# Kernel tuning notes

Measured on AMD Instinct MI355X. Metric: run time of the kernel, lower is better.

## Reference

```python
import jax, jax.numpy as jnp
import numpy as np

B, S = 2, 2048
DIM_IN, DIM_OUT, NUM_HEADS, DIM_QK = 1024, 128, 16, 128


def setup_inputs() -> dict:
    key = jax.random.key(0)
    k0, k1, k2, k3 = jax.random.split(key, 4)
    x = jax.random.normal(k0, (B, S, DIM_IN), jnp.float32)
    mask = jax.random.bernoulli(k1, 0.1, (B, S))  # True = masked-out token
    # xavier-normal-ish scales (exact init values are irrelevant for correctness)
    std_in = float(np.sqrt(2.0 / (NUM_HEADS * DIM_QK + DIM_IN * DIM_QK)))
    proj_in = jax.random.normal(k2, (DIM_IN, NUM_HEADS, 2 * DIM_QK + DIM_OUT), jnp.float32) * std_in
    v_bias = jnp.zeros((NUM_HEADS, DIM_OUT), jnp.float32)
    std_out = float(np.sqrt(2.0 / (DIM_OUT * DIM_OUT + NUM_HEADS * DIM_OUT)))
    proj_out = jax.random.normal(k3, (NUM_HEADS, DIM_OUT, DIM_OUT), jnp.float32) * std_out
    proj_out_bias = jnp.zeros((DIM_OUT,), jnp.float32)
    return {"x": x, "mask": mask, "proj_in": proj_in, "v_bias": v_bias,
            "proj_out": proj_out, "proj_out_bias": proj_out_bias}


def _rotary(t):
    # t: [z, s, h, d]; GPT-NeoX style rotary as in the torch Rotary module
    d = t.shape[-1]
    half = -(-d // 2)  # ceil(d/2), matches torch.arange(0,-1,-2/d)
    freq_half = 10000.0 ** (jnp.arange(half, dtype=jnp.float32) * (-2.0 / d))
    freq = jnp.concatenate([freq_half, freq_half[: half - d % 2]])  # length d
    pos = jnp.arange(t.shape[1], dtype=jnp.float32)
    ang = pos[:, None] * freq[None, :]             # [s, d]
    cos = jnp.cos(ang)[None, :, None, :]
    sin = jnp.sin(ang)[None, :, None, :]
    x1, x2 = jnp.split(t, 2, axis=-1)
    rot = jnp.concatenate([-x2, x1], axis=-1)
    return t * cos + rot * sin


def _inf_cube(t):
    return t ** 3


def reference(x, mask, proj_in, v_bias, proj_out, proj_out_bias):
    qkv = jnp.einsum('zki,iho->zkho', x, proj_in)
    q, k, v = jnp.split(qkv, [DIM_QK, 2 * DIM_QK], axis=-1)
    q = _rotary(q)
    k = _rotary(k)
    scores = jnp.einsum('zqha,zkha->zqkh', q, k) / jnp.sqrt(jnp.float32(DIM_QK))
    # dual mask: row (query) OR column (key) masked -> -inf
    m = jnp.logical_or(mask[:, :, None, None], mask[:, None, :, None])  # [z,q,k,1]
    scores = jnp.where(m, -jnp.inf, scores)
    attn = jnp.nan_to_num(jax.nn.softmax(scores, axis=2))  # softmax over k; nan rows -> 0
    o = jnp.einsum('zqkh,zkhx->zqhx', attn, v + v_bias[None, None])
    out = jnp.einsum('zqhx,hxy->zqy', _inf_cube(o), proj_out) + proj_out_bias[None, None]
    return _inf_cube(out)
```

## Files before the change

### kernel.cpp

```cpp
#include <hip/hip_runtime.h>
#include <math.h>

#define BZ 2
#define SQ 2048
#define DIN 1024
#define HH 16
#define NT 6144
#define MROWS 4096
#define KOUT 2048
#define KSPLIT 16

typedef unsigned short u16t;
typedef unsigned int u32t;
typedef __attribute__((ext_vector_type(8))) short bf16x8;
typedef __attribute__((ext_vector_type(4))) float f32x4;

__device__ __forceinline__ float cubef(float x) { return x * x * x; }

__device__ __forceinline__ u16t f2bf(float f) {
    u32t b = __float_as_uint(f);
    b += 0x7FFFu + ((b >> 16) & 1u);
    return (u16t)(b >> 16);
}
__device__ __forceinline__ float bf2f(u16t u) { return __uint_as_float(((u32t)u) << 16); }
__device__ __forceinline__ u32t pk2(float a, float b) {
    return (u32t)f2bf(a) | ((u32t)f2bf(b) << 16);
}

__global__ __launch_bounds__(256) void bf16_x(const float* __restrict__ x,
                                              u16t* __restrict__ xb) {
    const size_t idx = ((size_t)blockIdx.x * 256 + threadIdx.x) * 8;
    float4 f0 = *(const float4*)&x[idx];
    float4 f1 = *(const float4*)&x[idx + 4];
    u32t h[4];
    h[0] = pk2(f0.x, f0.y); h[1] = pk2(f0.z, f0.w);
    h[2] = pk2(f1.x, f1.y); h[3] = pk2(f1.z, f1.w);
    *(uint4*)&xb[idx] = *(uint4*)&h[0];
}

__global__ __launch_bounds__(256) void transpose_w(const float* __restrict__ W,
                                                   u16t* __restrict__ Th) {
    __shared__ float tile[64][68];
    const int n0 = blockIdx.x * 64;
    const int k0 = blockIdx.y * 64;
    const int t = threadIdx.x;
    {
        const int r = t >> 4, c = (t & 15) * 4;
        #pragma unroll
        for (int p = 0; p < 4; p++) {
            float4 v = *(const float4*)&W[(size_t)(k0 + r + p * 16) * NT + n0 + c];
            *(float4*)&tile[r + p * 16][c] = v;
        }
    }
    __syncthreads();
    const int nr = t >> 2;
    const int kc = (t & 3) * 16;
    u32t hi[8];
    #pragma unroll
    for (int j = 0; j < 8; j++)
        hi[j] = pk2(tile[kc + 2 * j][nr], tile[kc + 2 * j + 1][nr]);
    size_t ob = (size_t)(n0 + nr) * DIN + k0 + kc;
    *(uint4*)&Th[ob]     = *(uint4*)&hi[0];
    *(uint4*)&Th[ob + 8] = *(uint4*)&hi[4];
}

__global__ __launch_bounds__(256) void transpose_w2(const float* __restrict__ W,
                                                    u16t* __restrict__ Th) {
    __shared__ float tile[64][68];
    const int n0 = blockIdx.x * 64;
    const int k0 = blockIdx.y * 64;
    const int t = threadIdx.x;
    {
        const int r = t >> 4, c = (t & 15) * 4;
        #pragma unroll
        for (int p = 0; p < 4; p++) {
            float4 v = *(const float4*)&W[(size_t)(k0 + r + p * 16) * 128 + n0 + c];
            *(float4*)&tile[r + p * 16][c] = v;
        }
    }
    __syncthreads();
    const int nr = t >> 2;
    const int kc = (t & 3) * 16;
    u32t hi[8];
    #pragma unroll
    for (int j = 0; j < 8; j++)
        hi[j] = pk2(tile[kc + 2 * j][nr], tile[kc + 2 * j + 1][nr]);
    size_t ob = (size_t)(n0 + nr) * KOUT + k0 + kc;
    *(uint4*)&Th[ob]     = *(uint4*)&hi[0];
    *(uint4*)&Th[ob + 8] = *(uint4*)&hi[4];
}

__global__ __launch_bounds__(256) void gemm_qkv4(const u16t* __restrict__ Ah,
                                                 const u16t* __restrict__ Bh,
                                                 const float* __restrict__ vb,
                                                 u16t* __restrict__ QB,
                                                 u16t* __restrict__ KB,
                                                 u16t* __restrict__ VF) {
    __shared__ __align__(16) u16t as_h[2][4 * 128 * 8];
    __shared__ __align__(16) u16t bs_h[2][4 * 128 * 8];

    const int t = threadIdx.x;
    const int lane = t & 63, wid = t >> 6;
    const int quad = lane >> 4, l15 = lane & 15;
    const int wm = (wid & 1) * 64;
    const int wn = (wid >> 1) * 64;
    const int tile = blockIdx.x;
    const int h = tile / 3, t3 = tile - h * 3;
    const int colBase = tile * 128;
    const int rowBase = blockIdx.y * 128;
    const int sm = t & 127;
    const int skh = t >> 7;

    f32x4 acc[4][4];
    #pragma unroll
    for (int i = 0; i < 4; i++)
        #pragma unroll
        for (int j = 0; j < 4; j++) acc[i][j] = (f32x4){0.f, 0.f, 0.f, 0.f};

    const u16t* aPtr = Ah + (size_t)(rowBase + sm) * DIN + skh * 16;
    const u16t* bPtr = Bh + (size_t)(colBase + sm) * DIN + skh * 16;
    const int swoff = (skh * 2) * 1024 + sm * 8;

    uint4 a0 = *(const uint4*)(aPtr);
    uint4 a1 = *(const uint4*)(aPtr + 8);
    uint4 b0 = *(const uint4*)(bPtr);
    uint4 b1 = *(const uint4*)(bPtr + 8);

    for (int it = 0; it < 32; it++) {
        const int buf = it & 1;
        *(uint4*)(&as_h[buf][swoff])        = a0;
        *(uint4*)(&as_h[buf][swoff + 1024]) = a1;
        *(uint4*)(&bs_h[buf][swoff])        = b0;
        *(uint4*)(&bs_h[buf][swoff + 1024]) = b1;
        __syncthreads();
        {
            const int k0 = (it < 31) ? (it + 1) * 32 : it * 32;
            a0 = *(const uint4*)(aPtr + k0);
            a1 = *(const uint4*)(aPtr + k0 + 8);
            b0 = *(const uint4*)(bPtr + k0);
            b1 = *(const uint4*)(bPtr + k0 + 8);
        }
        bf16x8 ah[4], bh[4];
        #pragma unroll
        for (int mt = 0; mt < 4; mt++)
            ah[mt] = *(const bf16x8*)&as_h[buf][quad * 1024 + (wm + mt * 16 + l15) * 8];
        #pragma unroll
        for (int nt = 0; nt < 4; nt++)
            bh[nt] = *(const bf16x8*)&bs_h[buf][quad * 1024 + (wn + nt * 16 + l15) * 8];
        #pragma unroll
        for (int mt = 0; mt < 4; mt++)
            #pragma unroll
            for (int nt = 0; nt < 4; nt++)
                acc[mt][nt] = __builtin_amdgcn_mfma_f32_16x16x32_bf16(ah[mt], bh[nt], acc[mt][nt], 0, 0, 0);
    }

    const int z = rowBase >> 11;
    const int s0 = (rowBase & 2047) + wm + quad * 4;
    const size_t obase = (size_t)(z * 16 + h) * 2048;
    if (t3 == 2) {
        #pragma unroll
        for (int nt = 0; nt < 4; nt++) {
            int c = wn + nt * 16 + l15;
            float bb = vb[h * 128 + c];
            #pragma unroll
            for (int mt = 0; mt < 4; mt++)
                #pragma unroll
                for (int r = 0; r < 4; r++)
                    VF[(obase + s0 + mt * 16 + r) * 128 + c] = f2bf(acc[mt][nt][r] + bb);
        }
    } else {
        u16t* dst = t3 ? KB : QB;
        #pragma unroll
        for (int nt = 0; nt < 4; nt++) {
            int c = wn + nt * 16 + l15;
            #pragma unroll
            for (int mt = 0; mt < 4; mt++)
                #pragma unroll
                for (int r = 0; r < 4; r++)
                    dst[(obase + s0 + mt * 16 + r) * 128 + c] = f2bf(acc[mt][nt][r]);
        }
    }
}

__global__ __launch_bounds__(256) void prep_rot_trans(u16t* __restrict__ QB,
                                                      u16t* __restrict__ KB,
                                                      u16t* __restrict__ VTh) {
    const int bx = blockIdx.x;
    const int st = bx & 63, h = (bx >> 6) & 15, z = bx >> 10;
    const int t = threadIdx.x;
    const size_t base = ((size_t)(z * 16 + h) * 2048 + st * 32) * 128;

    {
        const int r = t >> 3, w = t & 7;
        const int c = w & 3;
        const int s = st * 32 + r;
        u16t* buf = (w < 4) ? QB : KB;
        u16t* p1 = buf + base + (size_t)r * 128 + c * 16;
        u16t* p2 = p1 + 64;
        uint4 a0 = *(uint4*)p1, a1 = *(uint4*)(p1 + 8);
        uint4 b0 = *(uint4*)p2, b1 = *(uint4*)(p2 + 8);
        u32t A[8] = {a0.x, a0.y, a0.z, a0.w, a1.x, a1.y, a1.z, a1.w};
        u32t B[8] = {b0.x, b0.y, b0.z, b0.w, b1.x, b1.y, b1.z, b1.w};
        u32t OA[8], OB[8];
        #pragma unroll
        for (int p = 0; p < 8; p++) {
            float x1a = bf2f((u16t)(A[p] & 0xFFFFu)), x1b = bf2f((u16t)(A[p] >> 16));
            float x2a = bf2f((u16t)(B[p] & 0xFFFFu)), x2b = bf2f((u16t)(B[p] >> 16));
            int j0 = c * 16 + 2 * p;
            float f0 = expf(-0.14391156831212788f * (float)j0);
            float f1 = expf(-0.14391156831212788f * (float)(j0 + 1));
            float sn0, cs0, sn1, cs1;
            sincosf((float)s * f0, &sn0, &cs0);
            sincosf((float)s * f1, &sn1, &cs1);
            OA[p] = pk2(x1a * cs0 - x2a * sn0, x1b * cs1 - x2b * sn1);
            OB[p] = pk2(x2a * cs0 + x1a * sn0, x2b * cs1 + x1b * sn1);
        }
        *(uint4*)p1       = make_uint4(OA[0], OA[1], OA[2], OA[3]);
        *(uint4*)(p1 + 8) = make_uint4(OA[4], OA[5], OA[6], OA[7]);
        *(uint4*)p2       = make_uint4(OB[0], OB[1], OB[2], OB[3]);
        *(uint4*)(p2 + 8) = make_uint4(OB[4], OB[5], OB[6], OB[7]);
    }

    __shared__ u16t vt[128 * 40];
    {
        uint4 a = *(uint4*)(VTh + base + t * 16);
        uint4 b = *(uint4*)(VTh + base + t * 16 + 8);
        int row = t >> 3, d0 = (t & 7) * 16;
        u32t W[8] = {a.x, a.y, a.z, a.w, b.x, b.y, b.z, b.w};
        #pragma unroll
        for (int p = 0; p < 8; p++) {
            vt[(d0 + 2 * p) * 40 + row]     = (u16t)(W[p] & 0xFFFFu);
            vt[(d0 + 2 * p + 1) * 40 + row] = (u16t)(W[p] >> 16);
        }
    }
    __syncthreads();
    {
        int d = t >> 1, k0 = (t & 1) * 16;
        uint4 a = *(uint4*)&vt[d * 40 + k0];
        uint4 b = *(uint4*)&vt[d * 40 + k0 + 8];
        *(uint4*)(VTh + base + t * 16)     = a;
        *(uint4*)(VTh + base + t * 16 + 8) = b;
    }
}

#define ATTSCALE 0.08838834764831845f

__global__ __launch_bounds__(256, 2) void attn_kernel7(const u16t* __restrict__ QB,
                                                       const u16t* __restrict__ KB,
                                                       const u16t* __restrict__ VTh,
                                                       const int* __restrict__ mask,
                                                       u16t* __restrict__ O3b) {
    const int blk = blockIdx.x;
    const int qt = blk & 15;
    const int h  = (blk >> 4) & 15;
    const int z  = blk >> 8;
    const int t  = threadIdx.x;
    const int lane = t & 63, wid = t >> 6;
    const int quad = lane >> 4, l15 = lane & 15;

    __shared__ __align__(16) u16t ks[2][32 * 136];
    __shared__ __align__(16) u16t vth[2][128 * 40];
    __shared__ __align__(16) u16t wlb[128 * 40];
    __shared__ int qm[128], km[2][32];

    const int q0 = qt * 128;
    const size_t zh = (size_t)(z * 16 + h);
    const u16t* qb  = QB  + zh * 262144;
    const u16t* kb  = KB  + zh * 262144;
    const u16t* vhg = VTh + zh * 262144;

    bf16x8 qf[2][4];
    #pragma unroll
    for (int i = 0; i < 2; i++)
        #pragma unroll
        for (int kk = 0; kk < 4; kk++)
            qf[i][kk] = *(const bf16x8*)(qb + (size_t)(q0 + 16 * (2 * wid + i) + l15) * 128 + kk * 32 + quad * 8);
    if (t < 128) qm[t] = mask[z * SQ + q0 + t];

    const int srow = t >> 3, sco = (t & 7) * 16;
    const int sdd = t >> 1, sk0 = (t & 1) * 16;

    uint4 ka, kb2, va, vb2;
    int kmv = 0;
    {
        ka  = *(const uint4*)(kb + t * 16);
        kb2 = *(const uint4*)(kb + t * 16 + 8);
        va  = *(const uint4*)(vhg + t * 16);
        vb2 = *(const uint4*)(vhg + t * 16 + 8);
        if (t < 32) kmv = mask[z * SQ + t];
    }

    f32x4 acc[2][8];
    #pragma unroll
    for (int i = 0; i < 2; i++)
        #pragma unroll
        for (int d = 0; d < 8; d++) acc[i][d] = (f32x4){0.f, 0.f, 0.f, 0.f};
    float dsum[2][4] = {{0.f, 0.f, 0.f, 0.f}, {0.f, 0.f, 0.f, 0.f}};

    for (int it = 0; it < 64; it++) {
        const int buf = it & 1;
        *(uint4*)&ks[buf][srow * 136 + sco]     = ka;
        *(uint4*)&ks[buf][srow * 136 + sco + 8] = kb2;
        *(uint4*)&vth[buf][sdd * 40 + sk0]      = va;
        *(uint4*)&vth[buf][sdd * 40 + sk0 + 8]  = vb2;
        if (t < 32) km[buf][t] = kmv;

        __syncthreads();

        {
            const int ktn = (it < 63) ? (it + 1) * 32 : it * 32;
            const u16t* src = kb + (size_t)ktn * 128 + t * 16;
            ka  = *(const uint4*)(src);
            kb2 = *(const uint4*)(src + 8);
            const u16t* srch = vhg + (size_t)(ktn >> 5) * 4096 + t * 16;
            va  = *(const uint4*)(srch);
            vb2 = *(const uint4*)(srch + 8);
            if (t < 32) kmv = mask[z * SQ + ktn + t];
        }

        f32x4 s4[2][2];
        #pragma unroll
        for (int i = 0; i < 2; i++)
            #pragma unroll
            for (int n = 0; n < 2; n++) s4[i][n] = (f32x4){0.f, 0.f, 0.f, 0.f};
        #pragma unroll
        for (int kk = 0; kk < 4; kk++) {
            bf16x8 kf0 = *(const bf16x8*)&ks[buf][l15 * 136 + kk * 32 + quad * 8];
            bf16x8 kf1 = *(const bf16x8*)&ks[buf][(16 + l15) * 136 + kk * 32 + quad * 8];
            s4[0][0] = __builtin_amdgcn_mfma_f32_16x16x32_bf16(qf[0][kk], kf0, s4[0][0], 0, 0, 0);
            s4[0][1] = __builtin_amdgcn_mfma_f32_16x16x32_bf16(qf[0][kk], kf1, s4[0][1], 0, 0, 0);
            s4[1][0] = __builtin_amdgcn_mfma_f32_16x16x32_bf16(qf[1][kk], kf0, s4[1][0], 0, 0, 0);
            s4[1][1] = __builtin_amdgcn_mfma_f32_16x16x32_bf16(qf[1][kk], kf1, s4[1][1], 0, 0, 0);
        }
        {
            int colm0 = km[buf][l15], colm1 = km[buf][16 + l15];
            #pragma unroll
            for (int i = 0; i < 2; i++)
                #pragma unroll
                for (int r = 0; r < 4; r++) {
                    int row = 16 * (2 * wid + i) + 4 * quad + r;
                    int qmr = qm[row];
                    float w0 = (qmr | colm0) ? 0.f : __expf(s4[i][0][r] * ATTSCALE);
                    float w1 = (qmr | colm1) ? 0.f : __expf(s4[i][1][r] * ATTSCALE);
                    dsum[i][r] += w0 + w1;
                    wlb[row * 40 + l15]      = f2bf(w0);
                    wlb[row * 40 + 16 + l15] = f2bf(w1);
                }
        }
        bf16x8 pa[2];
        #pragma unroll
        for (int i = 0; i < 2; i++)
            pa[i] = *(const bf16x8*)&wlb[(16 * (2 * wid + i) + l15) * 40 + quad * 8];
        #pragma unroll
        for (int dt = 0; dt < 8; dt++) {
            bf16x8 vh = *(const bf16x8*)&vth[buf][(16 * dt + l15) * 40 + quad * 8];
            acc[0][dt] = __builtin_amdgcn_mfma_f32_16x16x32_bf16(pa[0], vh, acc[0][dt], 0, 0, 0);
            acc[1][dt] = __builtin_amdgcn_mfma_f32_16x16x32_bf16(pa[1], vh, acc[1][dt], 0, 0, 0);
        }
    }

    #pragma unroll
    for (int i = 0; i < 2; i++)
        #pragma unroll
        for (int r = 0; r < 4; r++) {
            float v = dsum[i][r];
            v += __shfl_xor(v, 1);
            v += __shfl_xor(v, 2);
            v += __shfl_xor(v, 4);
            v += __shfl_xor(v, 8);
            dsum[i][r] = v;
        }

    #pragma unroll
    for (int i = 0; i < 2; i++)
        #pragma unroll
        for (int r = 0; r < 4; r++) {
            int row = 16 * (2 * wid + i) + 4 * quad + r;
            float inv = dsum[i][r] > 0.f ? 1.f / dsum[i][r] : 0.f;
            u16t* dst = O3b + (size_t)(z * SQ + q0 + row) * KOUT + h * 128;
            #pragma unroll
            for (int dt = 0; dt < 8; dt++)
                dst[16 * dt + l15] = f2bf(cubef(acc[i][dt][r] * inv));
        }
}

__global__ __launch_bounds__(256) void final_gemm3(const u16t* __restrict__ Ab,
                                                   const u16t* __restrict__ Bh,
                                                   float* __restrict__ part) {
    __shared__ __align__(16) u16t as_h[2][4 * 128 * 8];
    __shared__ __align__(16) u16t bs_h[2][4 * 128 * 8];

    const int t = threadIdx.x;
    const int lane = t & 63, wid = t >> 6;
    const int quad = lane >> 4, l15 = lane & 15;
    const int wm = (wid & 1) * 64;
    const int wn = (wid >> 1) * 64;
    const int rowBase = blockIdx.x * 128;
    const int kBase   = blockIdx.y * (KOUT / KSPLIT);
    const int sm = t & 127;
    const int skh = t >> 7;

    f32x4 acc[4][4];
    #pragma unroll
    for (int i = 0; i < 4; i++)
        #pragma unroll
        for (int j = 0; j < 4; j++) acc[i][j] = (f32x4){0.f, 0.f, 0.f, 0.f};

    const u16t* aPtr = Ab + (size_t)(rowBase + sm) * KOUT + kBase + skh * 16;
    const u16t* bPtr = Bh + (size_t)sm * KOUT + kBase + skh * 16;
    const int swoff = (skh * 2) * 1024 + sm * 8;

    uint4 a0 = *(const uint4*)(aPtr);
    uint4 a1 = *(const uint4*)(aPtr + 8);
    uint4 b0 = *(const uint4*)(bPtr);
    uint4 b1 = *(const uint4*)(bPtr + 8);

    const int NIT = (KOUT / KSPLIT) / 32;
    for (int it = 0; it < NIT; it++) {
        const int buf = it & 1;
        *(uint4*)(&as_h[buf][swoff])        = a0;
        *(uint4*)(&as_h[buf][swoff + 1024]) = a1;
        *(uint4*)(&bs_h[buf][swoff])        = b0;
        *(uint4*)(&bs_h[buf][swoff + 1024]) = b1;
        __syncthreads();
        {
            const int k0 = (it < NIT - 1) ? (it + 1) * 32 : it * 32;
            a0 = *(const uint4*)(aPtr + k0);
            a1 = *(const uint4*)(aPtr + k0 + 8);
            b0 = *(const uint4*)(bPtr + k0);
            b1 = *(const uint4*)(bPtr + k0 + 8);
        }
        bf16x8 ah[4], bh[4];
        #pragma unroll
        for (int mt = 0; mt < 4; mt++)
            ah[mt] = *(const bf16x8*)&as_h[buf][quad * 1024 + (wm + mt * 16 + l15) * 8];
        #pragma unroll
        for (int nt = 0; nt < 4; nt++)
            bh[nt] = *(const bf16x8*)&bs_h[buf][quad * 1024 + (wn + nt * 16 + l15) * 8];
        #pragma unroll
        for (int mt = 0; mt < 4; mt++)
            #pragma unroll
            for (int nt = 0; nt < 4; nt++)
                acc[mt][nt] = __builtin_amdgcn_mfma_f32_16x16x32_bf16(ah[mt], bh[nt], acc[mt][nt], 0, 0, 0);
    }

    float* pbase = part + (size_t)blockIdx.y * ((size_t)MROWS * 128);
    #pragma unroll
    for (int mt = 0; mt < 4; mt++)
        #pragma unroll
        for (int nt = 0; nt < 4; nt++) {
            int col = wn + nt * 16 + l15;
            #pragma unroll
            for (int r = 0; r < 4; r++) {
                int row = rowBase + wm + mt * 16 + quad * 4 + r;
                pbase[(size_t)row * 128 + col] = acc[mt][nt][r];
            }
        }
}

__global__ __launch_bounds__(256) void reduce_bias_cube(const float* __restrict__ part,
                                                        const float* __restrict__ bias,
                                                        float* __restrict__ out) {
    const int idx = (blockIdx.x * 256 + threadIdx.x) * 4;
    float4 s = {0.f, 0.f, 0.f, 0.f};
    #pragma unroll
    for (int p = 0; p < KSPLIT; p++) {
        float4 v = *(const float4*)&part[(size_t)p * ((size_t)MROWS * 128) + idx];
        s.x += v.x; s.y += v.y; s.z += v.z; s.w += v.w;
    }
    float4 b = *(const float4*)&bias[idx & 127];
    float4 r;
    r.x = cubef(s.x + b.x);
    r.y = cubef(s.y + b.y);
    r.z = cubef(s.z + b.z);
    r.w = cubef(s.w + b.w);
    *(float4*)&out[idx] = r;
}

extern "C" void kernel_launch(void* const* d_in, const int* in_sizes, int n_in,
                              void* d_out, int out_size, void* d_ws, size_t ws_size,
                              hipStream_t stream) {
    const float* x        = (const float*)d_in[0];
    const int*   mask     = (const int*)d_in[1];
    const float* proj_in  = (const float*)d_in[2];
    const float* v_bias   = (const float*)d_in[3];
    const float* proj_out = (const float*)d_in[4];
    const float* po_bias  = (const float*)d_in[5];
    float* out = (float*)d_out;

    u16t* QB  = (u16t*)d_ws;
    u16t* KB  = QB + (size_t)8388608;
    u16t* VTh = KB + (size_t)8388608;
    u16t* xb  = VTh + (size_t)8388608;
    u16t* O3b = xb + (size_t)4194304;
    u16t* pTh = O3b;
    u16t* WTh = QB;
    float* partials = (float*)(WTh + (size_t)128 * KOUT);

    bf16_x<<<(MROWS * DIN) / (256 * 8), 256, 0, stream>>>(x, xb);
    transpose_w<<<dim3(NT / 64, DIN / 64), 256, 0, stream>>>(proj_in, pTh);
    gemm_qkv4<<<dim3(48, MROWS / 128), 256, 0, stream>>>(xb, pTh, v_bias, QB, KB, VTh);
    prep_rot_trans<<<BZ * HH * (SQ / 32), 256, 0, stream>>>(QB, KB, VTh);
    attn_kernel7<<<BZ * HH * (SQ / 128), 256, 0, stream>>>(QB, KB, VTh, mask, O3b);
    transpose_w2<<<dim3(2, KOUT / 64), 256, 0, stream>>>(proj_out, WTh);
    final_gemm3<<<dim3(MROWS / 128, KSPLIT), 256, 0, stream>>>(O3b, WTh, partials);
    reduce_bias_cube<<<(MROWS * 128) / (256 * 4), 256, 0, stream>>>(partials, po_bias, out);
}
```

Baseline: 329.4 us.

## Use direct global-to-LDS loads in QKV GEMM and exp2 softmax with prescaled Q

```diff
diff --git a/kernel.cpp b/kernel.cpp
--- a/kernel.cpp
+++ b/kernel.cpp
@@ -25,6 +25,17 @@
 __device__ __forceinline__ float bf2f(u16t u) { return __uint_as_float(((u32t)u) << 16); }
 __device__ __forceinline__ u32t pk2(float a, float b) {
     return (u32t)f2bf(a) | ((u32t)f2bf(b) << 16);
+}
+
+#if __has_builtin(__builtin_amdgcn_exp2f)
+#define EXP2(x) __builtin_amdgcn_exp2f(x)
+#else
+#define EXP2(x) exp2f(x)
+#endif
+
+__device__ __forceinline__ void load_lds16(const void* g, void* l) {
+    __builtin_amdgcn_global_load_lds((const __attribute__((address_space(1))) void*)g,
+                                     (__attribute__((address_space(3))) void*)l, 16, 0, 0);
 }
 
 __global__ __launch_bounds__(256) void bf16_x(const float* __restrict__ x,
@@ -96,8 +107,8 @@
                                                  u16t* __restrict__ QB,
                                                  u16t* __restrict__ KB,
                                                  u16t* __restrict__ VF) {
-    __shared__ __align__(16) u16t as_h[2][4 * 128 * 8];
-    __shared__ __align__(16) u16t bs_h[2][4 * 128 * 8];
+    __shared__ __align__(16) u16t as_h[2][4096];
+    __shared__ __align__(16) u16t bs_h[2][4096];
 
     const int t = threadIdx.x;
     const int lane = t & 63, wid = t >> 6;
@@ -119,26 +130,22 @@
 
     const u16t* aPtr = Ah + (size_t)(rowBase + sm) * DIN + skh * 16;
     const u16t* bPtr = Bh + (size_t)(colBase + sm) * DIN + skh * 16;
-    const int swoff = (skh * 2) * 1024 + sm * 8;
-
-    uint4 a0 = *(const uint4*)(aPtr);
-    uint4 a1 = *(const uint4*)(aPtr + 8);
-    uint4 b0 = *(const uint4*)(bPtr);
-    uint4 b1 = *(const uint4*)(bPtr + 8);
+    const int wbase = (wid >> 1) * 2048 + (wid & 1) * 512;
+
+    load_lds16(aPtr,     &as_h[0][wbase]);
+    load_lds16(aPtr + 8, &as_h[0][wbase + 1024]);
+    load_lds16(bPtr,     &bs_h[0][wbase]);
+    load_lds16(bPtr + 8, &bs_h[0][wbase + 1024]);
 
     for (int it = 0; it < 32; it++) {
         const int buf = it & 1;
-        *(uint4*)(&as_h[buf][swoff])        = a0;
-        *(uint4*)(&as_h[buf][swoff + 1024]) = a1;
-        *(uint4*)(&bs_h[buf][swoff])        = b0;
-        *(uint4*)(&bs_h[buf][swoff + 1024]) = b1;
         __syncthreads();
-        {
-            const int k0 = (it < 31) ? (it + 1) * 32 : it * 32;
-            a0 = *(const uint4*)(aPtr + k0);
-            a1 = *(const uint4*)(aPtr + k0 + 8);
-            b0 = *(const uint4*)(bPtr + k0);
-            b1 = *(const uint4*)(bPtr + k0 + 8);
+        if (it < 31) {
+            const int k0 = (it + 1) * 32;
+            load_lds16(aPtr + k0,     &as_h[buf ^ 1][wbase]);
+            load_lds16(aPtr + k0 + 8, &as_h[buf ^ 1][wbase + 1024]);
+            load_lds16(bPtr + k0,     &bs_h[buf ^ 1][wbase]);
+            load_lds16(bPtr + k0 + 8, &bs_h[buf ^ 1][wbase + 1024]);
         }
         bf16x8 ah[4], bh[4];
         #pragma unroll
@@ -152,6 +159,7 @@
             #pragma unroll
             for (int nt = 0; nt < 4; nt++)
                 acc[mt][nt] = __builtin_amdgcn_mfma_f32_16x16x32_bf16(ah[mt], bh[nt], acc[mt][nt], 0, 0, 0);
+        __syncthreads();
     }
 
     const int z = rowBase >> 11;
@@ -181,6 +189,8 @@
         }
     }
 }
+
+#define QSC 0.12751744f
 
 __global__ __launch_bounds__(256) void prep_rot_trans(u16t* __restrict__ QB,
                                                       u16t* __restrict__ KB,
@@ -195,6 +205,7 @@
         const int c = w & 3;
         const int s = st * 32 + r;
         u16t* buf = (w < 4) ? QB : KB;
+        const float sc = (w < 4) ? QSC : 1.0f;
         u16t* p1 = buf + base + (size_t)r * 128 + c * 16;
         u16t* p2 = p1 + 64;
         uint4 a0 = *(uint4*)p1, a1 = *(uint4*)(p1 + 8);
@@ -212,6 +223,7 @@
             float sn0, cs0, sn1, cs1;
             sincosf((float)s * f0, &sn0, &cs0);
             sincosf((float)s * f1, &sn1, &cs1);
+            sn0 *= sc; cs0 *= sc; sn1 *= sc; cs1 *= sc;
             OA[p] = pk2(x1a * cs0 - x2a * sn0, x1b * cs1 - x2b * sn1);
             OB[p] = pk2(x2a * cs0 + x1a * sn0, x2b * cs1 + x1b * sn1);
         }
@@ -226,11 +238,12 @@
         uint4 a = *(uint4*)(VTh + base + t * 16);
         uint4 b = *(uint4*)(VTh + base + t * 16 + 8);
         int row = t >> 3, d0 = (t & 7) * 16;
+        int prow = 2 * (row & 15) + (row >> 4);
         u32t W[8] = {a.x, a.y, a.z, a.w, b.x, b.y, b.z, b.w};
         #pragma unroll
         for (int p = 0; p < 8; p++) {
-            vt[(d0 + 2 * p) * 40 + row]     = (u16t)(W[p] & 0xFFFFu);
-            vt[(d0 + 2 * p + 1) * 40 + row] = (u16t)(W[p] >> 16);
+            vt[(d0 + 2 * p) * 40 + prow]     = (u16t)(W[p] & 0xFFFFu);
+            vt[(d0 + 2 * p + 1) * 40 + prow] = (u16t)(W[p] >> 16);
         }
     }
     __syncthreads();
@@ -243,9 +256,7 @@
     }
 }
 
-#define ATTSCALE 0.08838834764831845f
-
-__global__ __launch_bounds__(256, 2) void attn_kernel7(const u16t* __restrict__ QB,
+__global__ __launch_bounds__(256, 2) void attn_kernel8(const u16t* __restrict__ QB,
                                                        const u16t* __restrict__ KB,
                                                        const u16t* __restrict__ VTh,
                                                        const int* __restrict__ mask,
@@ -261,7 +272,7 @@
     __shared__ __align__(16) u16t ks[2][32 * 136];
     __shared__ __align__(16) u16t vth[2][128 * 40];
     __shared__ __align__(16) u16t wlb[128 * 40];
-    __shared__ int qm[128], km[2][32];
+    __shared__ int km[2][32];
 
     const int q0 = qt * 128;
     const size_t zh = (size_t)(z * 16 + h);
@@ -275,7 +286,16 @@
         #pragma unroll
         for (int kk = 0; kk < 4; kk++)
             qf[i][kk] = *(const bf16x8*)(qb + (size_t)(q0 + 16 * (2 * wid + i) + l15) * 128 + kk * 32 + quad * 8);
-    if (t < 128) qm[t] = mask[z * SQ + q0 + t];
+
+    int4 qm4[2];
+    #pragma unroll
+    for (int i = 0; i < 2; i++)
+        qm4[i] = *(const int4*)&mask[z * SQ + q0 + 16 * (2 * wid + i) + 4 * quad];
+    const int qmr[2][4] = {{qm4[0].x, qm4[0].y, qm4[0].z, qm4[0].w},
+                           {qm4[1].x, qm4[1].y, qm4[1].z, qm4[1].w}};
+    int rowoff[2];
+    #pragma unroll
+    for (int i = 0; i < 2; i++) rowoff[i] = (16 * (2 * wid + i) + 4 * quad) * 40;
 
     const int srow = t >> 3, sco = (t & 7) * 16;
     const int sdd = t >> 1, sk0 = (t & 1) * 16;
@@ -338,13 +358,12 @@
             for (int i = 0; i < 2; i++)
                 #pragma unroll
                 for (int r = 0; r < 4; r++) {
-                    int row = 16 * (2 * wid + i) + 4 * quad + r;
-                    int qmr = qm[row];
-                    float w0 = (qmr | colm0) ? 0.f : __expf(s4[i][0][r] * ATTSCALE);
-                    float w1 = (qmr | colm1) ? 0.f : __expf(s4[i][1][r] * ATTSCALE);
+                    float w0 = (qmr[i][r] | colm0) ? 0.f : EXP2(s4[i][0][r]);
+                    float w1 = (qmr[i][r] | colm1) ? 0.f : EXP2(s4[i][1][r]);
                     dsum[i][r] += w0 + w1;
-                    wlb[row * 40 + l15]      = f2bf(w0);
-                    wlb[row * 40 + 16 + l15] = f2bf(w1);
+                    u32t pkw;
+                    asm("v_cvt_pk_bf16_f32 %0, %1, %2" : "=v"(pkw) : "v"(w0), "v"(w1));
+                    *(u32t*)&wlb[rowoff[i] + r * 40 + 2 * l15] = pkw;
                 }
         }
         bf16x8 pa[2];
@@ -501,7 +520,7 @@
     transpose_w<<<dim3(NT / 64, DIN / 64), 256, 0, stream>>>(proj_in, pTh);
     gemm_qkv4<<<dim3(48, MROWS / 128), 256, 0, stream>>>(xb, pTh, v_bias, QB, KB, VTh);
     prep_rot_trans<<<BZ * HH * (SQ / 32), 256, 0, stream>>>(QB, KB, VTh);
-    attn_kernel7<<<BZ * HH * (SQ / 128), 256, 0, stream>>>(QB, KB, VTh, mask, O3b);
+    attn_kernel8<<<BZ * HH * (SQ / 128), 256, 0, stream>>>(QB, KB, VTh, mask, O3b);
     transpose_w2<<<dim3(2, KOUT / 64), 256, 0, stream>>>(proj_out, WTh);
     final_gemm3<<<dim3(MROWS / 128, KSPLIT), 256, 0, stream>>>(O3b, WTh, partials);
     reduce_bias_cube<<<(MROWS * 128) / (256 * 4), 256, 0, stream>>>(partials, po_bias, out);
```

Result: faster. 319.9 us (-2.9%).
